# Kernel tuning notes

Hardware: AMD Instinct MI355X
Metric: run time of the kernel (lower is better)

Reference implementation:

```python
import jax, jax.numpy as jnp
import numpy as np

INPUT_DIM = 8192
HIDDEN = 512
EMBED = HIDDEN // 2  # op embedding dim
NUM_TEMPERS = 64
NUM_OPS = 3
MAX_HOPS = 4
B = 2048


def setup_inputs() -> dict:
    key = jax.random.key(0)
    ks = jax.random.split(key, 10)
    n = lambda k, shape: jax.random.normal(k, shape, jnp.float32)
    return {
        "x": n(ks[0], (B, INPUT_DIM)),
        "op_emb": 0.01 * n(ks[1], (NUM_OPS, EMBED)),
        "op_logits": jnp.zeros((NUM_OPS,), jnp.float32),
        "id_embeds": 0.01 * n(ks[2], (128, 4)),
        "W1": n(ks[3], (HIDDEN + 4 + EMBED, HIDDEN)) / np.sqrt(HIDDEN + 4 + EMBED),
        "b1": jnp.zeros((HIDDEN,), jnp.float32),
        "W2": n(ks[4], (HIDDEN, HIDDEN)) / np.sqrt(HIDDEN),
        "b2": jnp.zeros((HIDDEN,), jnp.float32),
        "Wr1": n(ks[5], (HIDDEN + 4, 32)) / np.sqrt(HIDDEN + 4),
        "br1": jnp.zeros((32,), jnp.float32),
        "Wr2": n(ks[6], (32, NUM_TEMPERS + 1)) / np.sqrt(32),
        "br2": jnp.zeros((NUM_TEMPERS + 1,), jnp.float32),
        "Wp": n(ks[7], (HIDDEN, INPUT_DIM)) / np.sqrt(HIDDEN),
        "bp": jnp.zeros((INPUT_DIM,), jnp.float32),
        "tid_emb": 0.01 * n(ks[8], (NUM_TEMPERS, 4)),
        "rng_seed": 42,
    }


def reference(x, op_emb, op_logits, id_embeds, W1, b1, W2, b2, Wr1, br1, Wr2, br2, Wp, bp, tid_emb, rng_seed):
    Bx, D = x.shape
    # D is a multiple of HIDDEN here -> no padding branch needed
    num_patches = D // HIDDEN
    patch_states = x.reshape(Bx * num_patches, HIDDEN)
    N = patch_states.shape[0]

    rng = jax.random.key(rng_seed)
    rng, tk = jax.random.split(rng)
    patch_tempers = jax.random.randint(tk, (N,), 0, NUM_TEMPERS)
    patch_done = jnp.zeros((N,), bool)

    # Fixed-length unroll of the while_loop (max_hops=4). Early-exit only
    # differs if ALL patches stop early, which is vanishingly unlikely.
    for hop in range(MAX_HOPS):
        # --- gather active patches (inactive slots fill with index 0, as in original) ---
        active_idx = jnp.where(~patch_done, size=N, fill_value=0)[0]
        x_active = patch_states[active_idx]          # [N, HIDDEN]
        t_active = patch_tempers[active_idx]         # [N]
        # --- Temper: sample op per patch, embed, 2-layer relu MLP ---
        rng, ok = jax.random.split(rng)
        op_probs = jax.nn.softmax(op_logits)
        op_idx = jax.random.categorical(ok, jnp.log(op_probs), shape=(N,))
        x_aug = jnp.concatenate([x_active, id_embeds[t_active], op_emb[op_idx]], axis=-1)
        h = jax.nn.relu(x_aug @ W1 + b1)
        h = jax.nn.relu(h @ W2 + b2)                 # [N, HIDDEN]
        # --- scatter back updated states ---
        patch_states = patch_states.at[active_idx].set(h)
        # --- routing policy + categorical sampling of next temper / stop ---
        enriched = jnp.concatenate([h, tid_emb[t_active]], axis=-1)
        logits = jax.nn.relu(enriched @ Wr1 + br1) @ Wr2 + br2
        rng, sk = jax.random.split(rng)
        sampled = jax.random.categorical(sk, jax.nn.log_softmax(logits))
        stop = sampled == NUM_TEMPERS
        next_t = jnp.clip(sampled, 0, NUM_TEMPERS - 1)
        patch_tempers = patch_tempers.at[active_idx].set(next_t)
        patch_done = patch_done.at[active_idx].set(stop)

    latent = patch_states.reshape(Bx, num_patches, HIDDEN).mean(axis=1)  # [B, HIDDEN]
    pred = latent @ Wp + bp                                              # [B, INPUT_DIM]
    return latent, pred
```

## Files before the change

### kernel.cpp

```cpp
#include <hip/hip_runtime.h>
#include <cstdint>
#include <cstddef>


#define NPATCH 32768
#define NHOP 4
#define RSCALE 4096.0f
#define RINV   2.44140625e-4f

typedef unsigned short u16;
typedef __attribute__((ext_vector_type(8))) _Float16 half8;
typedef __attribute__((ext_vector_type(4))) float f32x4;

__device__ __forceinline__ uint32_t rotl32(uint32_t x, int r){ return (x<<r)|(x>>(32-r)); }

__device__ __forceinline__ void tf2x32(uint32_t k0, uint32_t k1, uint32_t x0, uint32_t x1,
                                       uint32_t& o0, uint32_t& o1){
  uint32_t k2 = k0 ^ k1 ^ 0x1BD11BDAu;
  x0 += k0; x1 += k1;
#define TFR(r) { x0 += x1; x1 = rotl32(x1,(r)); x1 ^= x0; }
  TFR(13) TFR(15) TFR(26) TFR(6)   x0 += k1; x1 += k2 + 1u;
  TFR(17) TFR(29) TFR(16) TFR(24)  x0 += k2; x1 += k0 + 2u;
  TFR(13) TFR(15) TFR(26) TFR(6)   x0 += k0; x1 += k1 + 3u;
  TFR(17) TFR(29) TFR(16) TFR(24)  x0 += k1; x1 += k2 + 4u;
  TFR(13) TFR(15) TFR(26) TFR(6)   x0 += k2; x1 += k0 + 5u;
#undef TFR
  o0 = x0; o1 = x1;
}

__device__ __forceinline__ uint32_t jbits32(uint32_t k0, uint32_t k1, uint32_t idx){
  uint32_t a, b; tf2x32(k0, k1, 0u, idx, a, b);
  return a ^ b;
}

__device__ __forceinline__ void jsplit(uint32_t& r0, uint32_t& r1, uint32_t& c0, uint32_t& c1){
  uint32_t n0, n1;
  tf2x32(r0, r1, 0u, 0u, n0, n1);
  tf2x32(r0, r1, 0u, 1u, c0, c1);
  r0 = n0; r1 = n1;
}

__device__ __forceinline__ float jgumbel(uint32_t bits){
  float f = __uint_as_float(0x3f800000u | (bits >> 9)) - 1.0f;
  float u = fmaxf(f, 1.17549435e-38f);
  return -logf(-logf(u));
}

union uhcv { _Float16 h; u16 u; };
__device__ __forceinline__ u16 f2h(float x){ uhcv t; t.h = (_Float16)x; return t.u; }
__device__ __forceinline__ float h2f(u16 b){ uhcv t; t.u = b; return (float)t.h; }
__device__ __forceinline__ void split2s(float v, u16& a0, u16& a1){
  a0 = f2h(v);
  a1 = f2h((v - h2f(a0)) * RSCALE);
}

__global__ void k_keys(const int* __restrict__ seed, const float* __restrict__ op_logits,
                       uint32_t* __restrict__ keys, float* __restrict__ logp3){
  if (threadIdx.x != 0 || blockIdx.x != 0) return;
  uint32_t r0 = 0u, r1 = (uint32_t)seed[0];
  uint32_t c0, c1;
  jsplit(r0, r1, c0, c1); keys[0] = c0; keys[1] = c1;
  for (int h = 0; h < NHOP; h++){
    jsplit(r0, r1, c0, c1); keys[2 + 4*h] = c0; keys[3 + 4*h] = c1;
    jsplit(r0, r1, c0, c1); keys[4 + 4*h] = c0; keys[5 + 4*h] = c1;
  }
  float l0 = op_logits[0], l1 = op_logits[1], l2 = op_logits[2];
  float mm = fmaxf(l0, fmaxf(l1, l2));
  float e0 = expf(l0-mm), e1 = expf(l1-mm), e2 = expf(l2-mm);
  float ssum = e0 + e1 + e2;
  logp3[0] = logf(e0/ssum); logp3[1] = logf(e1/ssum); logp3[2] = logf(e2/ssum);
}

__global__ __launch_bounds__(256)
void k_init(const uint32_t* __restrict__ keys, int* __restrict__ tempers, int* __restrict__ done){
  int i = blockIdx.x*256 + threadIdx.x;
  uint32_t b = jbits32(keys[0], keys[1], (uint32_t)(NPATCH + i));
  tempers[i] = (int)(b & 63u);
  done[i] = 0;
}

__global__ __launch_bounds__(256)
void k_precomp(const float* __restrict__ id_embeds, const float* __restrict__ op_emb,
               const float* __restrict__ tid_emb,
               const float* __restrict__ W1, const float* __restrict__ b1,
               const float* __restrict__ Wr1, const float* __restrict__ br1,
               float* __restrict__ idW, float* __restrict__ opWb, float* __restrict__ tidWb){
  int b = blockIdx.x, tid = threadIdx.x;
  if (b < 64){
    for (int j = tid; j < 512; j += 256){
      float v = 0.f;
      #pragma unroll
      for (int u = 0; u < 4; u++) v = fmaf(id_embeds[b*4+u], W1[(size_t)(512+u)*512 + j], v);
      idW[b*512 + j] = v;
    }
  } else if (b < 67){
    int o = b - 64;
    for (int j = tid; j < 512; j += 256){
      float v = b1[j];
      for (int u = 0; u < 256; u++) v = fmaf(op_emb[o*256+u], W1[(size_t)(516+u)*512 + j], v);
      opWb[o*512 + j] = v;
    }
  } else {
    for (int idx = tid; idx < 2048; idx += 256){
      int t = idx >> 5, c = idx & 31;
      float v = br1[c];
      #pragma unroll
      for (int u = 0; u < 4; u++) v = fmaf(tid_emb[t*4+u], Wr1[(512+u)*32 + c], v);
      tidWb[idx] = v;
    }
  }
}

__global__ __launch_bounds__(256)
void k_splitW(const float* __restrict__ W1, const float* __restrict__ W2,
              const float* __restrict__ Wp,
              u16* __restrict__ W1T, u16* __restrict__ W2T, u16* __restrict__ WpT){
  __shared__ float t[32][33];
  int blk = blockIdx.x;
  const float* src; u16* dst; int N; int deg; size_t pst; int tb;
  if (blk < 256){ src = W1; dst = W1T; N = 512; deg = 2; pst = (size_t)512*512; tb = blk; }
  else if (blk < 512){ src = W2; dst = W2T; N = 512; deg = 2; pst = (size_t)512*512; tb = blk - 256; }
  else { src = Wp; dst = WpT; N = 8192; deg = 1; pst = 0; tb = blk - 512; }
  int n0 = (tb >> 4)*32, k0 = (tb & 15)*32;
  int r = threadIdx.x >> 5, c = threadIdx.x & 31;
  for (int rr = r; rr < 32; rr += 8)
    t[rr][c] = src[(size_t)(k0+rr)*N + n0 + c];
  __syncthreads();
  for (int rr = r; rr < 32; rr += 8){
    float v = t[c][rr];
    size_t o = (size_t)(n0+rr)*512 + k0 + c;
    if (deg == 2){
      u16 a0, a1; split2s(v, a0, a1);
      dst[o] = a0; dst[pst + o] = a1;
    } else {
      dst[o] = f2h(v);
    }
  }
}

__global__ __launch_bounds__(256)
void k_xsplit(const float* __restrict__ x, u16* __restrict__ sP){
  size_t i = ((size_t)blockIdx.x*256 + threadIdx.x)*4;
  float4 v = *(const float4*)(x + i);
  ushort4 p0, p1;
  split2s(v.x, p0.x, p1.x); split2s(v.y, p0.y, p1.y);
  split2s(v.z, p0.z, p1.z); split2s(v.w, p0.w, p1.w);
  const size_t SP = (size_t)NPATCH*512;
  *(ushort4*)(sP + i) = p0; *(ushort4*)(sP + SP + i) = p1;
}

__global__ __launch_bounds__(1024)
void k_scan(const int* __restrict__ done, int* __restrict__ aidx, int* __restrict__ meta){
  __shared__ int cnt[1024];
  int tid = threadIdx.x;
  int base = tid * 32;
  unsigned flags = 0; int c = 0;
  #pragma unroll
  for (int i = 0; i < 32; i++){
    int f = (done[base + i] == 0);
    flags |= ((unsigned)f) << i;
    c += f;
  }
  cnt[tid] = c;
  __syncthreads();
  int val = c;
  for (int off = 1; off < 1024; off <<= 1){
    int v = (tid >= off) ? cnt[tid - off] : 0;
    __syncthreads();
    val += v; cnt[tid] = val;
    __syncthreads();
  }
  int pos = val - c;
  for (int i = 0; i < 32; i++){
    if ((flags >> i) & 1u) aidx[pos++] = base + i;
  }
  __syncthreads();
  int na = cnt[1023];
  for (int j = na + tid; j < NPATCH; j += 1024) aidx[j] = 0;
  if (tid == 0){
    meta[0] = na;
    meta[1] = (na < NPATCH) ? (NPATCH - 1) : 0;
  }
}

__global__ __launch_bounds__(256)
void k_gather(const int* __restrict__ aidx, const int* __restrict__ tempers,
              const uint32_t* __restrict__ keys, const float* __restrict__ logp3,
              int hop, int* __restrict__ t_act, int* __restrict__ op_idx){
  int s = blockIdx.x*256 + threadIdx.x;
  int p = aidx[s];
  t_act[s] = tempers[p];
  uint32_t k0 = keys[2 + 4*hop], k1 = keys[3 + 4*hop];
  float best = 0.f; int bi = 0;
  #pragma unroll
  for (int c = 0; c < 3; c++){
    float v = jgumbel(jbits32(k0, k1, (uint32_t)(3*s + c))) + logp3[c];
    if (c == 0 || v > best){ best = v; bi = c; }
  }
  op_idx[s] = bi;
}

template<int MODE, int DEG>
__global__ __launch_bounds__(256, 2)
void k_mgemm(const u16* __restrict__ Ap, const u16* __restrict__ Bp,
             float* __restrict__ outF, u16* __restrict__ outP,
             const int* __restrict__ aidx, const float* __restrict__ bias,
             const float* __restrict__ idW, const float* __restrict__ opWb,
             const int* __restrict__ t_act, const int* __restrict__ op_idx,
             int Ncols, size_t aStride, size_t bStride, size_t oStride){
  __shared__ u16 As[DEG*4096];
  __shared__ u16 Bs[DEG*4096];
  const int tid = threadIdx.x;
  const int L = tid & 63, w = tid >> 6;
  const int m0 = blockIdx.y*128, n0 = blockIdx.x*128;
  const int wr = w >> 1, wc = w & 1;

  const int SPW = DEG*4;
  const bool isA = (w < 2);
  const u16* gB = isA ? Ap : Bp;
  u16* lB = isA ? As : Bs;
  const size_t pstride = isA ? aStride : bStride;
  const u16* gseg[8];
  u16* lseg[8];
  #pragma unroll
  for (int q = 0; q < SPW; q++){
    int ss = (w & 1)*SPW + q;
    int p = ss >> 3, rb = ss & 7;
    int row16 = rb*16 + (L >> 2);
    int grow;
    if (isA) grow = (MODE == 1) ? aidx[m0 + row16] : (m0 + row16);
    else     grow = n0 + row16;
    int swz = (L & 3) ^ ((L >> 2) & 3);
    gseg[q] = gB + p*pstride + (size_t)grow*512 + swz*8;
    lseg[q] = lB + p*4096 + rb*512;
  }

  f32x4 accM[4][4], accR[4][4];
  #pragma unroll
  for (int i = 0; i < 4; i++)
    #pragma unroll
    for (int j = 0; j < 4; j++){ accM[i][j] = (f32x4)0.f; accR[i][j] = (f32x4)0.f; }

  const int rdsw = ((L >> 4) ^ (L & 3))*8;
  const int frow = L & 15;

  for (int kt = 0; kt < 16; kt++){
    __syncthreads();
    #pragma unroll
    for (int q = 0; q < SPW; q++)
      __builtin_amdgcn_global_load_lds(
        (const __attribute__((address_space(1))) void*)(const void*)(gseg[q] + kt*32),
        (__attribute__((address_space(3))) void*)(void*)lseg[q], 16, 0, 0);
    __syncthreads();
    #pragma unroll
    for (int pa = 0; pa < DEG; pa++){
      half8 af[4];
      #pragma unroll
      for (int i = 0; i < 4; i++)
        af[i] = *(const half8*)&As[pa*4096 + (wr*64 + i*16 + frow)*32 + rdsw];
      #pragma unroll
      for (int pb = 0; pb < DEG - pa; pb++){
        #pragma unroll
        for (int j = 0; j < 4; j++){
          half8 bf = *(const half8*)&Bs[pb*4096 + (wc*64 + j*16 + frow)*32 + rdsw];
          #pragma unroll
          for (int i = 0; i < 4; i++){
            if (pa + pb == 0)
              accM[i][j] = __builtin_amdgcn_mfma_f32_16x16x32_f16(af[i], bf, accM[i][j], 0, 0, 0);
            else
              accR[i][j] = __builtin_amdgcn_mfma_f32_16x16x32_f16(af[i], bf, accR[i][j], 0, 0, 0);
          }
        }
      }
    }
  }

  const int rbase = m0 + wr*64 + (L >> 4)*4;
  const int cbase = n0 + wc*64 + (L & 15);
  #pragma unroll
  for (int i = 0; i < 4; i++){
    #pragma unroll
    for (int reg = 0; reg < 4; reg++){
      int r = rbase + i*16 + reg;
      if (MODE == 1){
        int t = t_act[r], o = op_idx[r];
        #pragma unroll
        for (int j = 0; j < 4; j++){
          int c = cbase + j*16;
          float v = accM[i][j][reg] + RINV*accR[i][j][reg] + idW[t*512 + c] + opWb[o*512 + c];
          v = fmaxf(v, 0.f);
          u16 a0, a1; split2s(v, a0, a1);
          size_t off = (size_t)r*512 + c;
          outP[off] = a0; outP[oStride + off] = a1;
        }
      } else {
        #pragma unroll
        for (int j = 0; j < 4; j++){
          int c = cbase + j*16;
          float v = accM[i][j][reg] + bias[c];
          if (DEG == 2) v += RINV*accR[i][j][reg];
          if (MODE == 0) v = fmaxf(v, 0.f);
          outF[(size_t)r*Ncols + c] = v;
        }
      }
    }
  }
}

__global__ __launch_bounds__(256)
void k_route2(const float* __restrict__ h2, const float* __restrict__ Wr1,
              const float* __restrict__ Wr2, const float* __restrict__ br2,
              const float* __restrict__ tidWb,
              const int* __restrict__ t_act, const int* __restrict__ aidx,
              const int* __restrict__ meta, const uint32_t* __restrict__ keys, int hop,
              u16* __restrict__ sP, int* __restrict__ tempers, int* __restrict__ done){
  __shared__ float Wr1s[256][32];
  __shared__ float h2s[8][512];
  __shared__ float l32[8][32];

  const int tid = threadIdx.x;
  const int s0 = blockIdx.x * 8;

  for (int i4 = tid; i4 < 8*128; i4 += 256){
    int sl = i4 >> 7, q = i4 & 127;
    *(float4*)&h2s[sl][q*4] = *(const float4*)&h2[(size_t)(s0+sl)*512 + q*4];
  }

  const int lane = tid & 63, w = tid >> 6;
  const int half = lane >> 5, col = lane & 31;
  const int sl = w*2 + half;
  const int s  = s0 + sl;
  const int t  = t_act[s];
  float acc = tidWb[t*32 + col];

  for (int kh = 0; kh < 2; kh++){
    __syncthreads();
    for (int idx = tid; idx < 256*32; idx += 256)
      Wr1s[idx >> 5][idx & 31] = Wr1[kh*8192 + idx];
    __syncthreads();
    const int kb = kh * 256;
    #pragma unroll 4
    for (int k4 = 0; k4 < 64; k4++){
      float4 hv = *(float4*)&h2s[sl][kb + k4*4];
      acc = fmaf(hv.x, Wr1s[k4*4+0][col], acc);
      acc = fmaf(hv.y, Wr1s[k4*4+1][col], acc);
      acc = fmaf(hv.z, Wr1s[k4*4+2][col], acc);
      acc = fmaf(hv.w, Wr1s[k4*4+3][col], acc);
    }
  }
  l32[sl][col] = fmaxf(acc, 0.f);
  __syncthreads();

  const uint32_t sk0 = keys[4 + 4*hop], sk1 = keys[5 + 4*hop];
  int smp[2];
  for (int pass = 0; pass < 2; pass++){
    const int psl = w*2 + pass;
    const int ps  = s0 + psl;
    const int c = lane;
    float lg = br2[c];
    #pragma unroll
    for (int k = 0; k < 32; k++) lg = fmaf(l32[psl][k], Wr2[k*65 + c], lg);
    float lg64 = br2[64];
    #pragma unroll
    for (int k = 0; k < 32; k++) lg64 = fmaf(l32[psl][k], Wr2[k*65 + 64], lg64);
    float m = lg;
    for (int off = 32; off; off >>= 1) m = fmaxf(m, __shfl_xor(m, off));
    m = fmaxf(m, lg64);
    float se = expf(lg - m);
    for (int off = 32; off; off >>= 1) se += __shfl_xor(se, off);
    se += expf(lg64 - m);
    float Lse = logf(se);
    float g = jgumbel(jbits32(sk0, sk1, (uint32_t)(65*ps + c)));
    float v = (lg - m) - Lse + g;
    int idx = c;
    for (int off = 32; off; off >>= 1){
      float ov = __shfl_xor(v, off);
      int   oi = __shfl_xor(idx, off);
      if (ov > v || (ov == v && oi < idx)){ v = ov; idx = oi; }
    }
    float g64 = jgumbel(jbits32(sk0, sk1, (uint32_t)(65*ps + 64)));
    float v64 = (lg64 - m) - Lse + g64;
    if (v64 > v) idx = 64;
    smp[pass] = idx;
  }

  const int mysmp = smp[half];
  const int p = aidx[s];
  const int w0v = meta[1];
  const bool allowed = (p != 0) || (s == w0v);
  if (allowed){
    const size_t SP = (size_t)NPATCH*512;
    for (int q = col; q < 128; q += 32){
      float4 v = *(float4*)&h2s[sl][q*4];
      ushort4 p0, p1;
      split2s(v.x, p0.x, p1.x); split2s(v.y, p0.y, p1.y);
      split2s(v.z, p0.z, p1.z); split2s(v.w, p0.w, p1.w);
      size_t o = (size_t)p*512 + q*4;
      *(ushort4*)(sP + o) = p0; *(ushort4*)(sP + SP + o) = p1;
    }
    if (col == 0){
      tempers[p] = (mysmp < 63) ? mysmp : 63;
      done[p]    = (mysmp == 64) ? 1 : 0;
    }
  }
}

__global__ __launch_bounds__(256)
void k_latent2(const u16* __restrict__ sP, float* __restrict__ outF, u16* __restrict__ latP){
  int idx = blockIdx.x*256 + threadIdx.x;
  int b = idx >> 9, j = idx & 511;
  const size_t SP = (size_t)NPATCH*512;
  float s = 0.f;
  #pragma unroll 4
  for (int u = 0; u < 16; u++){
    size_t e = (size_t)(b*16 + u)*512 + j;
    s += h2f(sP[e]) + RINV*h2f(sP[SP + e]);
  }
  s *= 0.0625f;
  outF[idx] = s;
  latP[idx] = f2h(s);
}

template<int MODE>
__global__ __launch_bounds__(256)
void k_gemmF(const float* __restrict__ A, const float* __restrict__ B, float* __restrict__ C,
             int Ncols,
             const int* __restrict__ aidx,
             const float* __restrict__ bias,
             const float* __restrict__ idW, const float* __restrict__ opWb,
             const int* __restrict__ t_act, const int* __restrict__ op_idx){
  __shared__ float As[16][128];
  __shared__ float Bs[16][128];
  const int tid = threadIdx.x;
  const int bx = blockIdx.x, by = blockIdx.y;
  const int tx = tid & 15, ty = tid >> 4;
  const int lr = tid >> 1, lhalf = tid & 1;
  const int srow = by*128 + lr;
  const int arow = (MODE == 1) ? aidx[srow] : srow;
  const float* Ap = A + (size_t)arow*512 + lhalf*8;
  const float* Bp = B + (size_t)(tid >> 4)*Ncols + bx*128 + (tid & 15)*8;

  float acc[8][8];
  #pragma unroll
  for (int i = 0; i < 8; i++)
    #pragma unroll
    for (int j = 0; j < 8; j++) acc[i][j] = 0.f;

  for (int kt = 0; kt < 512; kt += 16){
    float4 a0 = *(const float4*)(Ap + kt);
    float4 a1 = *(const float4*)(Ap + kt + 4);
    float4 g0 = *(const float4*)(Bp + (size_t)kt*Ncols);
    float4 g1 = *(const float4*)(Bp + (size_t)kt*Ncols + 4);
    __syncthreads();
    As[lhalf*8+0][lr] = a0.x; As[lhalf*8+1][lr] = a0.y;
    As[lhalf*8+2][lr] = a0.z; As[lhalf*8+3][lr] = a0.w;
    As[lhalf*8+4][lr] = a1.x; As[lhalf*8+5][lr] = a1.y;
    As[lhalf*8+6][lr] = a1.z; As[lhalf*8+7][lr] = a1.w;
    *(float4*)&Bs[tid>>4][(tid&15)*8]     = g0;
    *(float4*)&Bs[tid>>4][(tid&15)*8 + 4] = g1;
    __syncthreads();
    #pragma unroll
    for (int k = 0; k < 16; k++){
      float4 av0 = *(float4*)&As[k][ty*8];
      float4 av1 = *(float4*)&As[k][ty*8+4];
      float4 bv0 = *(float4*)&Bs[k][tx*4];
      float4 bv1 = *(float4*)&Bs[k][64 + tx*4];
      float av[8] = {av0.x,av0.y,av0.z,av0.w,av1.x,av1.y,av1.z,av1.w};
      float bv[8] = {bv0.x,bv0.y,bv0.z,bv0.w,bv1.x,bv1.y,bv1.z,bv1.w};
      #pragma unroll
      for (int i = 0; i < 8; i++)
        #pragma unroll
        for (int j = 0; j < 8; j++)
          acc[i][j] = fmaf(av[i], bv[j], acc[i][j]);
    }
  }

  const int col0a = bx*128 + tx*4;
  const int col0b = col0a + 64;
  #pragma unroll
  for (int i = 0; i < 8; i++){
    int s = by*128 + ty*8 + i;
    float adda[4], addb[4];
    if (MODE == 1){
      int t = t_act[s], o = op_idx[s];
      float4 ia = *(const float4*)&idW[t*512 + col0a];
      float4 ib = *(const float4*)&idW[t*512 + col0b];
      float4 oa = *(const float4*)&opWb[o*512 + col0a];
      float4 ob = *(const float4*)&opWb[o*512 + col0b];
      adda[0]=ia.x+oa.x; adda[1]=ia.y+oa.y; adda[2]=ia.z+oa.z; adda[3]=ia.w+oa.w;
      addb[0]=ib.x+ob.x; addb[1]=ib.y+ob.y; addb[2]=ib.z+ob.z; addb[3]=ib.w+ob.w;
    } else {
      float4 ba = *(const float4*)&bias[col0a];
      float4 bb = *(const float4*)&bias[col0b];
      adda[0]=ba.x; adda[1]=ba.y; adda[2]=ba.z; adda[3]=ba.w;
      addb[0]=bb.x; addb[1]=bb.y; addb[2]=bb.z; addb[3]=bb.w;
    }
    float4 va, vb;
    float* pa = &va.x; float* pb = &vb.x;
    #pragma unroll
    for (int j = 0; j < 4; j++){
      float v0 = acc[i][j]   + adda[j];
      float v1 = acc[i][j+4] + addb[j];
      if (MODE != 2){ v0 = fmaxf(v0, 0.f); v1 = fmaxf(v1, 0.f); }
      pa[j] = v0; pb[j] = v1;
    }
    *(float4*)(C + (size_t)s*Ncols + col0a) = va;
    *(float4*)(C + (size_t)s*Ncols + col0b) = vb;
  }
}

__global__ __launch_bounds__(256)
void k_routeF(const float* __restrict__ h2, const float* __restrict__ Wr1,
              const float* __restrict__ Wr2, const float* __restrict__ br2,
              const float* __restrict__ tidWb,
              const int* __restrict__ t_act, const int* __restrict__ aidx,
              const int* __restrict__ meta, const uint32_t* __restrict__ keys, int hop,
              float* __restrict__ states, int* __restrict__ tempers, int* __restrict__ done){
  __shared__ float Wr1s[256][32];
  __shared__ float h2s[8][512];
  __shared__ float l32[8][32];

  const int tid = threadIdx.x;
  const int s0 = blockIdx.x * 8;

  for (int i4 = tid; i4 < 8*128; i4 += 256){
    int sl = i4 >> 7, q = i4 & 127;
    *(float4*)&h2s[sl][q*4] = *(const float4*)&h2[(size_t)(s0+sl)*512 + q*4];
  }

  const int lane = tid & 63, w = tid >> 6;
  const int half = lane >> 5, col = lane & 31;
  const int sl = w*2 + half;
  const int s  = s0 + sl;
  const int t  = t_act[s];
  float acc = tidWb[t*32 + col];

  for (int kh = 0; kh < 2; kh++){
    __syncthreads();
    for (int idx = tid; idx < 256*32; idx += 256)
      Wr1s[idx >> 5][idx & 31] = Wr1[kh*8192 + idx];
    __syncthreads();
    const int kb = kh * 256;
    #pragma unroll 4
    for (int k4 = 0; k4 < 64; k4++){
      float4 hv = *(float4*)&h2s[sl][kb + k4*4];
      acc = fmaf(hv.x, Wr1s[k4*4+0][col], acc);
      acc = fmaf(hv.y, Wr1s[k4*4+1][col], acc);
      acc = fmaf(hv.z, Wr1s[k4*4+2][col], acc);
      acc = fmaf(hv.w, Wr1s[k4*4+3][col], acc);
    }
  }
  l32[sl][col] = fmaxf(acc, 0.f);
  __syncthreads();

  const uint32_t sk0 = keys[4 + 4*hop], sk1 = keys[5 + 4*hop];
  int smp[2];
  for (int pass = 0; pass < 2; pass++){
    const int psl = w*2 + pass;
    const int ps  = s0 + psl;
    const int c = lane;
    float lg = br2[c];
    #pragma unroll
    for (int k = 0; k < 32; k++) lg = fmaf(l32[psl][k], Wr2[k*65 + c], lg);
    float lg64 = br2[64];
    #pragma unroll
    for (int k = 0; k < 32; k++) lg64 = fmaf(l32[psl][k], Wr2[k*65 + 64], lg64);
    float m = lg;
    for (int off = 32; off; off >>= 1) m = fmaxf(m, __shfl_xor(m, off));
    m = fmaxf(m, lg64);
    float se = expf(lg - m);
    for (int off = 32; off; off >>= 1) se += __shfl_xor(se, off);
    se += expf(lg64 - m);
    float Lse = logf(se);
    float g = jgumbel(jbits32(sk0, sk1, (uint32_t)(65*ps + c)));
    float v = (lg - m) - Lse + g;
    int idx = c;
    for (int off = 32; off; off >>= 1){
      float ov = __shfl_xor(v, off);
      int   oi = __shfl_xor(idx, off);
      if (ov > v || (ov == v && oi < idx)){ v = ov; idx = oi; }
    }
    float g64 = jgumbel(jbits32(sk0, sk1, (uint32_t)(65*ps + 64)));
    float v64 = (lg64 - m) - Lse + g64;
    if (v64 > v) idx = 64;
    smp[pass] = idx;
  }

  const int mysmp = smp[half];
  const int p = aidx[s];
  const int w0v = meta[1];
  const bool allowed = (p != 0) || (s == w0v);
  if (allowed){
    const float4* src = (const float4*)&h2s[sl][0];
    float4* dst = (float4*)(states + (size_t)p*512);
    for (int q = col; q < 128; q += 32) dst[q] = src[q];
    if (col == 0){
      tempers[p] = (mysmp < 63) ? mysmp : 63;
      done[p]    = (mysmp == 64) ? 1 : 0;
    }
  }
}

__global__ __launch_bounds__(256)
void k_latentF(const float* __restrict__ states, float* __restrict__ out){
  int idx = blockIdx.x*256 + threadIdx.x;
  int b = idx >> 9, j = idx & 511;
  float s = 0.f;
  #pragma unroll
  for (int u = 0; u < 16; u++) s += states[(size_t)(b*16 + u)*512 + j];
  out[idx] = s * 0.0625f;
}

extern "C" void kernel_launch(void* const* d_in, const int* in_sizes, int n_in,
                              void* d_out, int out_size, void* d_ws, size_t ws_size,
                              hipStream_t stream) {
  (void)in_sizes; (void)n_in; (void)out_size;
  const float* x         = (const float*)d_in[0];
  const float* op_emb    = (const float*)d_in[1];
  const float* op_logits = (const float*)d_in[2];
  const float* id_embeds = (const float*)d_in[3];
  const float* W1        = (const float*)d_in[4];
  const float* b1        = (const float*)d_in[5];
  const float* W2        = (const float*)d_in[6];
  const float* b2        = (const float*)d_in[7];
  const float* Wr1       = (const float*)d_in[8];
  const float* br1       = (const float*)d_in[9];
  const float* Wr2       = (const float*)d_in[10];
  const float* br2       = (const float*)d_in[11];
  const float* Wp        = (const float*)d_in[12];
  const float* bp        = (const float*)d_in[13];
  const float* tid_emb   = (const float*)d_in[14];
  const int*   seed      = (const int*)d_in[15];
  float* out = (float*)d_out;

  char* w = (char*)d_ws;
  uint32_t* keys = (uint32_t*)w;
  float* logp3   = (float*)(w + 256);
  int*   meta    = (int*)(w + 512);
  int*   tempers = (int*)(w + 4096);
  int*   done    = tempers + NPATCH;
  int*   t_act   = done + NPATCH;
  int*   op_idx  = t_act + NPATCH;
  int*   aidx    = op_idx + NPATCH;
  float* idW     = (float*)(aidx + NPATCH);
  float* opWb    = idW + 64*512;
  float* tidWb   = opWb + 3*512;

  const size_t SPh = (size_t)NPATCH*512;
  u16* W1T     = (u16*)(w + (1u<<20));
  u16* W2T     = W1T + (size_t)2*512*512;
  u16* WpT     = W2T + (size_t)2*512*512;
  u16* latP    = WpT + (size_t)8192*512;
  u16* statesP = latP + (size_t)2048*512;
  u16* h1P     = statesP + 2*SPh;
  float* h2W   = (float*)(h1P + 2*SPh);
  const size_t NEED1 = (size_t)((char*)(h2W) - w);
  const size_t NEED2 = NEED1 + SPh*sizeof(float);

  k_keys<<<1, 64, 0, stream>>>(seed, op_logits, keys, logp3);
  k_init<<<NPATCH/256, 256, 0, stream>>>(keys, tempers, done);
  k_precomp<<<68, 256, 0, stream>>>(id_embeds, op_emb, tid_emb, W1, b1, Wr1, br1,
                                    idW, opWb, tidWb);

  if (ws_size >= NEED2){
    float* h2 = h2W;
    k_splitW<<<4608, 256, 0, stream>>>(W1, W2, Wp, W1T, W2T, WpT);
    k_xsplit<<<(NPATCH*512/4)/256, 256, 0, stream>>>(x, statesP);

    for (int hop = 0; hop < NHOP; hop++){
      k_scan<<<1, 1024, 0, stream>>>(done, aidx, meta);
      k_gather<<<NPATCH/256, 256, 0, stream>>>(aidx, tempers, keys, logp3, hop, t_act, op_idx);
      k_mgemm<1,2><<<dim3(4, NPATCH/128), 256, 0, stream>>>(
          statesP, W1T, nullptr, h1P, aidx, nullptr, idW, opWb, t_act, op_idx,
          512, SPh, (size_t)512*512, SPh);
      k_mgemm<0,2><<<dim3(4, NPATCH/128), 256, 0, stream>>>(
          h1P, W2T, h2, nullptr, nullptr, b2, nullptr, nullptr, nullptr, nullptr,
          512, SPh, (size_t)512*512, 0);
      k_route2<<<NPATCH/8, 256, 0, stream>>>(h2, Wr1, Wr2, br2, tidWb, t_act, aidx,
                                             meta, keys, hop, statesP, tempers, done);
    }

    k_latent2<<<(2048*512)/256, 256, 0, stream>>>(statesP, out, latP);
    k_mgemm<2,1><<<dim3(64, 16), 256, 0, stream>>>(
        latP, WpT, out + 2048*512, nullptr, nullptr, bp, nullptr, nullptr, nullptr, nullptr,
        8192, (size_t)2048*512, (size_t)8192*512, 0);
  } else {
    const size_t BIG0 = 2u<<20;
    const size_t SB   = (size_t)NPATCH * 512 * sizeof(float);
    float *states, *h1, *h2;
    bool copy_states;
    if (ws_size >= BIG0 + 3*SB){
      states = (float*)(w + BIG0);
      h1     = (float*)(w + BIG0 + SB);
      h2     = (float*)(w + BIG0 + 2*SB);
      copy_states = true;
    } else {
      states = (float*)d_in[0];
      h1     = (float*)(w + BIG0);
      h2     = (float*)(w + BIG0 + SB);
      copy_states = false;
    }
    if (copy_states)
      hipMemcpyAsync(states, x, SB, hipMemcpyDeviceToDevice, stream);

    for (int hop = 0; hop < NHOP; hop++){
      k_scan<<<1, 1024, 0, stream>>>(done, aidx, meta);
      k_gather<<<NPATCH/256, 256, 0, stream>>>(aidx, tempers, keys, logp3, hop, t_act, op_idx);
      k_gemmF<1><<<dim3(4, NPATCH/128), 256, 0, stream>>>(states, W1, h1, 512,
                                      aidx, nullptr, idW, opWb, t_act, op_idx);
      k_gemmF<0><<<dim3(4, NPATCH/128), 256, 0, stream>>>(h1, W2, h2, 512,
                                      nullptr, b2, nullptr, nullptr, nullptr, nullptr);
      k_routeF<<<NPATCH/8, 256, 0, stream>>>(h2, Wr1, Wr2, br2, tidWb, t_act, aidx,
                                      meta, keys, hop, states, tempers, done);
    }

    k_latentF<<<(2048*512)/256, 256, 0, stream>>>(states, out);
    k_gemmF<2><<<dim3(8192/128, 2048/128), 256, 0, stream>>>(out, Wp, out + 2048*512, 8192,
                                      nullptr, bp, nullptr, nullptr, nullptr, nullptr);
  }
}
```

Before: 1.210 ms.

## Fuse state scatter into second GEMM and move routing layer to MFMA

The second MLP GEMM now applies bias and ReLU and scatters the split-fp16 state directly into the patch-state buffer, so the fp32 h2 intermediate is no longer written and re-read. The routing first layer becomes a separate MFMA GEMM that reads the gathered split states against a pre-split Wr1, replacing the scalar FMA loop in k_route2. A small sampling kernel then does the second routing layer and categorical sampling. This adds one launch per hop and makes the routing GEMM depend on the scattered states, but cuts memory traffic and scalar compute.

```diff
diff --git a/kernel.cpp b/kernel.cpp
--- a/kernel.cpp
+++ b/kernel.cpp
@@ -11,6 +11,10 @@
 typedef unsigned short u16;
 typedef __attribute__((ext_vector_type(8))) _Float16 half8;
 typedef __attribute__((ext_vector_type(4))) float f32x4;
+
+#define GLDS(gp, lp) __builtin_amdgcn_global_load_lds( \
+    (const __attribute__((address_space(1))) void*)(const void*)(gp), \
+    (__attribute__((address_space(3))) void*)(void*)(lp), 16, 0, 0)
 
 __device__ __forceinline__ uint32_t rotl32(uint32_t x, int r){ return (x<<r)|(x>>(32-r)); }
 
@@ -113,20 +117,24 @@
 
 __global__ __launch_bounds__(256)
 void k_splitW(const float* __restrict__ W1, const float* __restrict__ W2,
-              const float* __restrict__ Wp,
-              u16* __restrict__ W1T, u16* __restrict__ W2T, u16* __restrict__ WpT){
+              const float* __restrict__ Wp, const float* __restrict__ Wr1,
+              u16* __restrict__ W1T, u16* __restrict__ W2T, u16* __restrict__ WpT,
+              u16* __restrict__ Wr1P){
   __shared__ float t[32][33];
   int blk = blockIdx.x;
   const float* src; u16* dst; int N; int deg; size_t pst; int tb;
   if (blk < 256){ src = W1; dst = W1T; N = 512; deg = 2; pst = (size_t)512*512; tb = blk; }
   else if (blk < 512){ src = W2; dst = W2T; N = 512; deg = 2; pst = (size_t)512*512; tb = blk - 256; }
-  else { src = Wp; dst = WpT; N = 8192; deg = 1; pst = 0; tb = blk - 512; }
+  else if (blk < 528){ src = Wr1; dst = Wr1P; N = 32; deg = 2; pst = (size_t)32*512; tb = blk - 512; }
+  else { src = Wp; dst = WpT; N = 8192; deg = 1; pst = 0; tb = blk - 528; }
   int n0 = (tb >> 4)*32, k0 = (tb & 15)*32;
+  if (N == 32){ n0 = 0; k0 = tb*32; }
   int r = threadIdx.x >> 5, c = threadIdx.x & 31;
   for (int rr = r; rr < 32; rr += 8)
-    t[rr][c] = src[(size_t)(k0+rr)*N + n0 + c];
+    t[rr][c] = src[(size_t)(k0+rr)*N + ((n0 + c) % N)];
   __syncthreads();
   for (int rr = r; rr < 32; rr += 8){
+    if (n0 + rr >= N) break;
     float v = t[c][rr];
     size_t o = (size_t)(n0+rr)*512 + k0 + c;
     if (deg == 2){
@@ -207,6 +215,7 @@
              const int* __restrict__ aidx, const float* __restrict__ bias,
              const float* __restrict__ idW, const float* __restrict__ opWb,
              const int* __restrict__ t_act, const int* __restrict__ op_idx,
+             const int* __restrict__ meta,
              int Ncols, size_t aStride, size_t bStride, size_t oStride){
   __shared__ u16 As[DEG*4096];
   __shared__ u16 Bs[DEG*4096];
@@ -248,9 +257,7 @@
     __syncthreads();
     #pragma unroll
     for (int q = 0; q < SPW; q++)
-      __builtin_amdgcn_global_load_lds(
-        (const __attribute__((address_space(1))) void*)(const void*)(gseg[q] + kt*32),
-        (__attribute__((address_space(3))) void*)(void*)lseg[q], 16, 0, 0);
+      GLDS(gseg[q] + kt*32, lseg[q]);
     __syncthreads();
     #pragma unroll
     for (int pa = 0; pa < DEG; pa++){
@@ -277,6 +284,7 @@
 
   const int rbase = m0 + wr*64 + (L >> 4)*4;
   const int cbase = n0 + wc*64 + (L & 15);
+  const int w0v = (MODE == 3) ? meta[1] : 0;
   #pragma unroll
   for (int i = 0; i < 4; i++){
     #pragma unroll
@@ -293,13 +301,26 @@
           size_t off = (size_t)r*512 + c;
           outP[off] = a0; outP[oStride + off] = a1;
         }
+      } else if (MODE == 3){
+        int p = aidx[r];
+        bool allowed = (p != 0) || (r == w0v);
+        #pragma unroll
+        for (int j = 0; j < 4; j++){
+          int c = cbase + j*16;
+          float v = accM[i][j][reg] + RINV*accR[i][j][reg] + bias[c];
+          v = fmaxf(v, 0.f);
+          if (allowed){
+            u16 a0, a1; split2s(v, a0, a1);
+            size_t off = (size_t)p*512 + c;
+            outP[off] = a0; outP[oStride + off] = a1;
+          }
+        }
       } else {
         #pragma unroll
         for (int j = 0; j < 4; j++){
           int c = cbase + j*16;
           float v = accM[i][j][reg] + bias[c];
           if (DEG == 2) v += RINV*accR[i][j][reg];
-          if (MODE == 0) v = fmaxf(v, 0.f);
           outF[(size_t)r*Ncols + c] = v;
         }
       }
@@ -307,50 +328,88 @@
   }
 }
 
-__global__ __launch_bounds__(256)
-void k_route2(const float* __restrict__ h2, const float* __restrict__ Wr1,
-              const float* __restrict__ Wr2, const float* __restrict__ br2,
-              const float* __restrict__ tidWb,
-              const int* __restrict__ t_act, const int* __restrict__ aidx,
-              const int* __restrict__ meta, const uint32_t* __restrict__ keys, int hop,
-              u16* __restrict__ sP, int* __restrict__ tempers, int* __restrict__ done){
-  __shared__ float Wr1s[256][32];
-  __shared__ float h2s[8][512];
-  __shared__ float l32[8][32];
-
+__global__ __launch_bounds__(256, 2)
+void k_routemm(const u16* __restrict__ sP, const u16* __restrict__ Wr1P,
+               const int* __restrict__ aidx, const int* __restrict__ t_act,
+               const float* __restrict__ tidWb, float* __restrict__ l32g){
+  __shared__ u16 As[2*2048];
+  __shared__ u16 Bs[2048];
+  const int tid = threadIdx.x;
+  const int L = tid & 63, w = tid >> 6;
+  const int m0 = blockIdx.x*64;
+  const size_t SPh = (size_t)NPATCH*512;
+
+  const u16* gseg[2]; u16* lseg[2];
+  #pragma unroll
+  for (int q = 0; q < 2; q++){
+    int ss = w*2 + q;
+    int p = ss >> 2, rb = ss & 3;
+    int row16 = rb*16 + (L >> 2);
+    int grow = aidx[m0 + row16];
+    int swz = (L & 3) ^ ((L >> 2) & 3);
+    gseg[q] = sP + p*SPh + (size_t)grow*512 + swz*8;
+    lseg[q] = As + p*2048 + rb*512;
+  }
+  const u16* gBp = Wr1P + (size_t)(tid>>7)*16384
+                        + (size_t)(((tid>>6)&1)*16 + (tid&15))*512 + ((tid>>4)&3)*8;
+  u16* lBp = Bs + w*512;
+
+  f32x4 accM[2], accR[2];
+  accM[0] = (f32x4)0.f; accM[1] = (f32x4)0.f;
+  accR[0] = (f32x4)0.f; accR[1] = (f32x4)0.f;
+
+  const int rdsw = ((L >> 4) ^ (L & 3))*8;
+  for (int kt = 0; kt < 16; kt++){
+    __syncthreads();
+    #pragma unroll
+    for (int q = 0; q < 2; q++)
+      GLDS(gseg[q] + kt*32, lseg[q]);
+    GLDS(gBp + kt*32, lBp);
+    __syncthreads();
+    #pragma unroll
+    for (int pa = 0; pa < 2; pa++){
+      half8 af = *(const half8*)&As[pa*2048 + (w*16 + (L & 15))*32 + rdsw];
+      #pragma unroll
+      for (int pb = 0; pb < 2 - pa; pb++){
+        #pragma unroll
+        for (int ct = 0; ct < 2; ct++){
+          half8 bf = *(const half8*)&Bs[(pb*2 + ct)*512 + (L >> 4)*128 + (L & 15)*8];
+          if (pa + pb == 0)
+            accM[ct] = __builtin_amdgcn_mfma_f32_16x16x32_f16(af, bf, accM[ct], 0, 0, 0);
+          else
+            accR[ct] = __builtin_amdgcn_mfma_f32_16x16x32_f16(af, bf, accR[ct], 0, 0, 0);
+        }
+      }
+    }
+  }
+
+  #pragma unroll
+  for (int reg = 0; reg < 4; reg++){
+    int s = m0 + w*16 + (L >> 4)*4 + reg;
+    int t = t_act[s];
+    #pragma unroll
+    for (int ct = 0; ct < 2; ct++){
+      int c = ct*16 + (L & 15);
+      float v = accM[ct][reg] + RINV*accR[ct][reg] + tidWb[t*32 + c];
+      l32g[(size_t)s*32 + c] = fmaxf(v, 0.f);
+    }
+  }
+}
+
+__global__ __launch_bounds__(256)
+void k_sample(const float* __restrict__ l32g, const float* __restrict__ Wr2,
+              const float* __restrict__ br2,
+              const int* __restrict__ aidx, const int* __restrict__ meta,
+              const uint32_t* __restrict__ keys, int hop,
+              int* __restrict__ tempers, int* __restrict__ done){
+  __shared__ float l32s[8][32];
   const int tid = threadIdx.x;
   const int s0 = blockIdx.x * 8;
-
-  for (int i4 = tid; i4 < 8*128; i4 += 256){
-    int sl = i4 >> 7, q = i4 & 127;
-    *(float4*)&h2s[sl][q*4] = *(const float4*)&h2[(size_t)(s0+sl)*512 + q*4];
-  }
+  l32s[tid >> 5][tid & 31] = l32g[(size_t)s0*32 + tid];
+  __syncthreads();
 
   const int lane = tid & 63, w = tid >> 6;
-  const int half = lane >> 5, col = lane & 31;
-  const int sl = w*2 + half;
-  const int s  = s0 + sl;
-  const int t  = t_act[s];
-  float acc = tidWb[t*32 + col];
-
-  for (int kh = 0; kh < 2; kh++){
-    __syncthreads();
-    for (int idx = tid; idx < 256*32; idx += 256)
-      Wr1s[idx >> 5][idx & 31] = Wr1[kh*8192 + idx];
-    __syncthreads();
-    const int kb = kh * 256;
-    #pragma unroll 4
-    for (int k4 = 0; k4 < 64; k4++){
-      float4 hv = *(float4*)&h2s[sl][kb + k4*4];
-      acc = fmaf(hv.x, Wr1s[k4*4+0][col], acc);
-      acc = fmaf(hv.y, Wr1s[k4*4+1][col], acc);
-      acc = fmaf(hv.z, Wr1s[k4*4+2][col], acc);
-      acc = fmaf(hv.w, Wr1s[k4*4+3][col], acc);
-    }
-  }
-  l32[sl][col] = fmaxf(acc, 0.f);
-  __syncthreads();
-
+  const int half = lane >> 5;
   const uint32_t sk0 = keys[4 + 4*hop], sk1 = keys[5 + 4*hop];
   int smp[2];
   for (int pass = 0; pass < 2; pass++){
@@ -359,10 +418,10 @@
     const int c = lane;
     float lg = br2[c];
     #pragma unroll
-    for (int k = 0; k < 32; k++) lg = fmaf(l32[psl][k], Wr2[k*65 + c], lg);
+    for (int k = 0; k < 32; k++) lg = fmaf(l32s[psl][k], Wr2[k*65 + c], lg);
     float lg64 = br2[64];
     #pragma unroll
-    for (int k = 0; k < 32; k++) lg64 = fmaf(l32[psl][k], Wr2[k*65 + 64], lg64);
+    for (int k = 0; k < 32; k++) lg64 = fmaf(l32s[psl][k], Wr2[k*65 + 64], lg64);
     float m = lg;
     for (int off = 32; off; off >>= 1) m = fmaxf(m, __shfl_xor(m, off));
     m = fmaxf(m, lg64);
@@ -384,24 +443,13 @@
     smp[pass] = idx;
   }
 
+  const int s = s0 + w*2 + half;
   const int mysmp = smp[half];
   const int p = aidx[s];
-  const int w0v = meta[1];
-  const bool allowed = (p != 0) || (s == w0v);
-  if (allowed){
-    const size_t SP = (size_t)NPATCH*512;
-    for (int q = col; q < 128; q += 32){
-      float4 v = *(float4*)&h2s[sl][q*4];
-      ushort4 p0, p1;
-      split2s(v.x, p0.x, p1.x); split2s(v.y, p0.y, p1.y);
-      split2s(v.z, p0.z, p1.z); split2s(v.w, p0.w, p1.w);
-      size_t o = (size_t)p*512 + q*4;
-      *(ushort4*)(sP + o) = p0; *(ushort4*)(sP + SP + o) = p1;
-    }
-    if (col == 0){
-      tempers[p] = (mysmp < 63) ? mysmp : 63;
-      done[p]    = (mysmp == 64) ? 1 : 0;
-    }
+  const bool allowed = (p != 0) || (s == meta[1]);
+  if (allowed && (lane & 31) == 0){
+    tempers[p] = (mysmp < 63) ? mysmp : 63;
+    done[p]    = (mysmp == 64) ? 1 : 0;
   }
 }
 
@@ -649,41 +697,41 @@
   const size_t SPh = (size_t)NPATCH*512;
   u16* W1T     = (u16*)(w + (1u<<20));
   u16* W2T     = W1T + (size_t)2*512*512;
-  u16* WpT     = W2T + (size_t)2*512*512;
+  u16* Wr1P    = W2T + (size_t)2*512*512;
+  u16* WpT     = Wr1P + (size_t)2*32*512;
   u16* latP    = WpT + (size_t)8192*512;
   u16* statesP = latP + (size_t)2048*512;
   u16* h1P     = statesP + 2*SPh;
-  float* h2W   = (float*)(h1P + 2*SPh);
-  const size_t NEED1 = (size_t)((char*)(h2W) - w);
-  const size_t NEED2 = NEED1 + SPh*sizeof(float);
+  float* l32g  = (float*)(h1P + 2*SPh);
+  const size_t NEED = (size_t)((char*)(l32g + (size_t)NPATCH*32) - w);
 
   k_keys<<<1, 64, 0, stream>>>(seed, op_logits, keys, logp3);
   k_init<<<NPATCH/256, 256, 0, stream>>>(keys, tempers, done);
   k_precomp<<<68, 256, 0, stream>>>(id_embeds, op_emb, tid_emb, W1, b1, Wr1, br1,
                                     idW, opWb, tidWb);
 
-  if (ws_size >= NEED2){
-    float* h2 = h2W;
-    k_splitW<<<4608, 256, 0, stream>>>(W1, W2, Wp, W1T, W2T, WpT);
+  if (ws_size >= NEED){
+    k_splitW<<<4624, 256, 0, stream>>>(W1, W2, Wp, Wr1, W1T, W2T, WpT, Wr1P);
     k_xsplit<<<(NPATCH*512/4)/256, 256, 0, stream>>>(x, statesP);
 
     for (int hop = 0; hop < NHOP; hop++){
       k_scan<<<1, 1024, 0, stream>>>(done, aidx, meta);
       k_gather<<<NPATCH/256, 256, 0, stream>>>(aidx, tempers, keys, logp3, hop, t_act, op_idx);
       k_mgemm<1,2><<<dim3(4, NPATCH/128), 256, 0, stream>>>(
-          statesP, W1T, nullptr, h1P, aidx, nullptr, idW, opWb, t_act, op_idx,
+          statesP, W1T, nullptr, h1P, aidx, nullptr, idW, opWb, t_act, op_idx, meta,
           512, SPh, (size_t)512*512, SPh);
-      k_mgemm<0,2><<<dim3(4, NPATCH/128), 256, 0, stream>>>(
-          h1P, W2T, h2, nullptr, nullptr, b2, nullptr, nullptr, nullptr, nullptr,
-          512, SPh, (size_t)512*512, 0);
-      k_route2<<<NPATCH/8, 256, 0, stream>>>(h2, Wr1, Wr2, br2, tidWb, t_act, aidx,
-                                             meta, keys, hop, statesP, tempers, done);
+      k_mgemm<3,2><<<dim3(4, NPATCH/128), 256, 0, stream>>>(
+          h1P, W2T, nullptr, statesP, aidx, b2, nullptr, nullptr, nullptr, nullptr, meta,
+          512, SPh, (size_t)512*512, SPh);
+      k_routemm<<<NPATCH/64, 256, 0, stream>>>(statesP, Wr1P, aidx, t_act, tidWb, l32g);
+      k_sample<<<NPATCH/8, 256, 0, stream>>>(l32g, Wr2, br2, aidx, meta, keys, hop,
+                                             tempers, done);
     }
 
     k_latent2<<<(2048*512)/256, 256, 0, stream>>>(statesP, out, latP);
     k_mgemm<2,1><<<dim3(64, 16), 256, 0, stream>>>(
         latP, WpT, out + 2048*512, nullptr, nullptr, bp, nullptr, nullptr, nullptr, nullptr,
-        8192, (size_t)2048*512, (size_t)8192*512, 0);
+        nullptr, 8192, (size_t)2048*512, (size_t)8192*512, 0);
   } else {
     const size_t BIG0 = 2u<<20;
     const size_t SB   = (size_t)NPATCH * 512 * sizeof(float);
```

Result: faster. 1.072 ms (-11.4%).
